# Optimization experiments

Measured on AMD Instinct MI355X. Metric: run time of the kernel, lower is better.

The kernel has to match this reference:

```python
import jax, jax.numpy as jnp
import numpy as np
import math

D_MODEL = 512


def setup_inputs() -> dict:
    key = jax.random.key(0)
    x = jax.random.normal(key, (16384, 32), dtype=jnp.float32)
    return {"x": x}


def reference(x) -> jnp.ndarray:
    # x: [B, F]; output: [B, D_MODEL]
    d_model = D_MODEL
    # div_term: [D/2]
    div_term = jnp.exp(jnp.arange(0, d_model, 2, dtype=jnp.float32) * (-(math.log(10000.0) / d_model)))
    # sinusoid input: [B, F, D/2]
    si = x[:, :, None] * div_term
    sin_mean = jnp.sin(si).mean(axis=1)  # [B, D/2]
    cos_mean = jnp.cos(si).mean(axis=1)  # [B, D/2]
    # interleave: out[:, 0::2] = sin_mean, out[:, 1::2] = cos_mean
    out = jnp.stack([sin_mean, cos_mean], axis=-1).reshape(x.shape[0], d_model)
    return out
```

## Files before the change

kernel.cpp:

```cpp
#include <hip/hip_runtime.h>

#define F 32
#define TPB 256
#define BLOCKS 2048

__device__ constexpr float kTable[14] = {
     3.125e-2f,
    -1.5625e-2f,
    -5.2083333333333e-3f,
     1.3020833333333e-3f,
     2.6041666666667e-4f,
    -4.3402777777778e-5f,
    -6.2003968253968e-6f,
     7.7504960317460e-7f,
     8.6116622574956e-8f,
    -8.6116622574956e-9f,
    -7.8287838704505e-10f,
     6.5239865587088e-11f,
     5.0184511989929e-12f,
    -3.5846079992806e-13f
};

#define DPP_ADD(x, ctrl)                                                                 \
    x += __int_as_float(__builtin_amdgcn_update_dpp(                                     \
        0, __float_as_int(x), (ctrl), 0xf, 0xf, true))

#define RDLANE(x, l) __int_as_float(__builtin_amdgcn_readlane(__float_as_int(x), (l)))

__global__ __launch_bounds__(TPB) void pe_kernel(const float* __restrict__ x,
                                                 float4* __restrict__ out,
                                                 int B) {
    const int lane = threadIdx.x & 63;
    const int fl   = lane & 31;
    const bool hi  = lane >= 32;
    const int gwave  = blockIdx.x * (TPB / 64) + (threadIdx.x >> 6);
    const int nwaves = gridDim.x * (TPB / 64);

    const float kExp = -0.05190512648261503f;

    float coef[7];
#pragma unroll
    for (int k = 0; k < 7; ++k) coef[k] = hi ? kTable[7 + k] : kTable[k];

    float d[4], t[4];
    d[0] = __builtin_amdgcn_exp2f((float)(2 * lane) * kExp);
    d[1] = __builtin_amdgcn_exp2f((float)(2 * lane + 1) * kExp);
    d[2] = d[0] * 0.01f;
    d[3] = d[1] * 0.01f;
#pragma unroll
    for (int m = 0; m < 4; ++m) t[m] = d[m] * d[m];

    for (int r = gwave; r < B; r += nwaves) {
        const float v = x[r * F + fl];
        const float v2 = v * v,   v3 = v2 * v,  v4 = v2 * v2,
                    v5 = v3 * v2, v6 = v3 * v3, v8 = v4 * v4;
        const float base = hi ? v8 : v;

        float rm[7];
        rm[0] = base * coef[0];
        rm[1] = (base * coef[1]) * v;
        rm[2] = (base * coef[2]) * v2;
        rm[3] = (base * coef[3]) * v3;
        rm[4] = (base * coef[4]) * v4;
        rm[5] = (base * coef[5]) * v5;
        rm[6] = (base * coef[6]) * v6;

#pragma unroll
        for (int k = 0; k < 7; ++k) {
            DPP_ADD(rm[k], 0x111);
            DPP_ADD(rm[k], 0x112);
            DPP_ADD(rm[k], 0x114);
            DPP_ADD(rm[k], 0x118);
            DPP_ADD(rm[k], 0x142);
        }

        const float M1  = RDLANE(rm[0], 31), M2  = RDLANE(rm[1], 31),
                    M3  = RDLANE(rm[2], 31), M4  = RDLANE(rm[3], 31),
                    M5  = RDLANE(rm[4], 31), M6  = RDLANE(rm[5], 31),
                    M7  = RDLANE(rm[6], 31),
                    M8  = RDLANE(rm[0], 63), M9  = RDLANE(rm[1], 63),
                    M10 = RDLANE(rm[2], 63), M11 = RDLANE(rm[3], 63),
                    M12 = RDLANE(rm[4], 63), M13 = RDLANE(rm[5], 63),
                    M14 = RDLANE(rm[6], 63);

        float4* orow = out + r * (512 / 4);
#pragma unroll
        for (int m = 0; m < 2; ++m) {
            const float ta = t[2 * m], tb = t[2 * m + 1];

            float s0 = M13;
            s0 = fmaf(s0, ta, M11); s0 = fmaf(s0, ta, M9);
            s0 = fmaf(s0, ta, M7);  s0 = fmaf(s0, ta, M5);
            s0 = fmaf(s0, ta, M3);  s0 = fmaf(s0, ta, M1);
            float c0 = M14;
            c0 = fmaf(c0, ta, M12); c0 = fmaf(c0, ta, M10);
            c0 = fmaf(c0, ta, M8);  c0 = fmaf(c0, ta, M6);
            c0 = fmaf(c0, ta, M4);  c0 = fmaf(c0, ta, M2);
            c0 = fmaf(c0, ta, 1.0f);

            float s1 = M13;
            s1 = fmaf(s1, tb, M11); s1 = fmaf(s1, tb, M9);
            s1 = fmaf(s1, tb, M7);  s1 = fmaf(s1, tb, M5);
            s1 = fmaf(s1, tb, M3);  s1 = fmaf(s1, tb, M1);
            float c1 = M14;
            c1 = fmaf(c1, tb, M12); c1 = fmaf(c1, tb, M10);
            c1 = fmaf(c1, tb, M8);  c1 = fmaf(c1, tb, M6);
            c1 = fmaf(c1, tb, M4);  c1 = fmaf(c1, tb, M2);
            c1 = fmaf(c1, tb, 1.0f);

            orow[lane + 64 * m] =
                make_float4(s0 * d[2 * m], c0, s1 * d[2 * m + 1], c1);
        }
    }
}

extern "C" void kernel_launch(void* const* d_in, const int* in_sizes, int n_in,
                              void* d_out, int out_size, void* d_ws, size_t ws_size,
                              hipStream_t stream) {
    const float* x = (const float*)d_in[0];
    float4* out = (float4*)d_out;
    const int B = in_sizes[0] / F;
    pe_kernel<<<BLOCKS, TPB, 0, stream>>>(x, out, B);
}
```

Before: 66.05 us.

## Use one wave per row, packed FMA Horner, and nontemporal stores

Replaces the grid-stride loop with one row per wave and doubles the block count to 4096 so the grid exactly covers B rows. The sin and cos Horner polynomials are paired into two-wide vector FMAs, which can map to packed FP32 FMA instructions. Output stores become nontemporal. The trade-off is that the per-lane setup (exp2 and coefficient selects) is now paid once per row instead of being amortized over several rows.

New measurement: 65.15 us. No clear change (-1.4%).

```diff
diff --git a/kernel.cpp b/kernel.cpp
--- a/kernel.cpp
+++ b/kernel.cpp
@@ -2,7 +2,10 @@
 
 #define F 32
 #define TPB 256
-#define BLOCKS 2048
+#define BLOCKS 4096
+
+typedef float f32x2 __attribute__((ext_vector_type(2)));
+typedef float f32x4 __attribute__((ext_vector_type(4)));
 
 __device__ constexpr float kTable[14] = {
      3.125e-2f,
@@ -28,13 +31,13 @@
 #define RDLANE(x, l) __int_as_float(__builtin_amdgcn_readlane(__float_as_int(x), (l)))
 
 __global__ __launch_bounds__(TPB) void pe_kernel(const float* __restrict__ x,
-                                                 float4* __restrict__ out,
+                                                 f32x4* __restrict__ out,
                                                  int B) {
     const int lane = threadIdx.x & 63;
     const int fl   = lane & 31;
     const bool hi  = lane >= 32;
-    const int gwave  = blockIdx.x * (TPB / 64) + (threadIdx.x >> 6);
-    const int nwaves = gridDim.x * (TPB / 64);
+    const int r    = blockIdx.x * (TPB / 64) + (threadIdx.x >> 6);
+    if (r >= B) return;
 
     const float kExp = -0.05190512648261503f;
 
@@ -50,67 +53,65 @@
 #pragma unroll
     for (int m = 0; m < 4; ++m) t[m] = d[m] * d[m];
 
-    for (int r = gwave; r < B; r += nwaves) {
-        const float v = x[r * F + fl];
-        const float v2 = v * v,   v3 = v2 * v,  v4 = v2 * v2,
-                    v5 = v3 * v2, v6 = v3 * v3, v8 = v4 * v4;
-        const float base = hi ? v8 : v;
+    const float v = x[r * F + fl];
+    const float v2 = v * v,   v3 = v2 * v,  v4 = v2 * v2,
+                v5 = v3 * v2, v6 = v3 * v3, v8 = v4 * v4;
+    const float base = hi ? v8 : v;
 
-        float rm[7];
-        rm[0] = base * coef[0];
-        rm[1] = (base * coef[1]) * v;
-        rm[2] = (base * coef[2]) * v2;
-        rm[3] = (base * coef[3]) * v3;
-        rm[4] = (base * coef[4]) * v4;
-        rm[5] = (base * coef[5]) * v5;
-        rm[6] = (base * coef[6]) * v6;
+    float rm[7];
+    rm[0] = base * coef[0];
+    rm[1] = (base * coef[1]) * v;
+    rm[2] = (base * coef[2]) * v2;
+    rm[3] = (base * coef[3]) * v3;
+    rm[4] = (base * coef[4]) * v4;
+    rm[5] = (base * coef[5]) * v5;
+    rm[6] = (base * coef[6]) * v6;
 
 #pragma unroll
-        for (int k = 0; k < 7; ++k) {
-            DPP_ADD(rm[k], 0x111);
-            DPP_ADD(rm[k], 0x112);
-            DPP_ADD(rm[k], 0x114);
-            DPP_ADD(rm[k], 0x118);
-            DPP_ADD(rm[k], 0x142);
-        }
+    for (int k = 0; k < 7; ++k) {
+        DPP_ADD(rm[k], 0x111);
+        DPP_ADD(rm[k], 0x112);
+        DPP_ADD(rm[k], 0x114);
+        DPP_ADD(rm[k], 0x118);
+        DPP_ADD(rm[k], 0x142);
+    }
 
-        const float M1  = RDLANE(rm[0], 31), M2  = RDLANE(rm[1], 31),
-                    M3  = RDLANE(rm[2], 31), M4  = RDLANE(rm[3], 31),
-                    M5  = RDLANE(rm[4], 31), M6  = RDLANE(rm[5], 31),
-                    M7  = RDLANE(rm[6], 31),
-                    M8  = RDLANE(rm[0], 63), M9  = RDLANE(rm[1], 63),
-                    M10 = RDLANE(rm[2], 63), M11 = RDLANE(rm[3], 63),
-                    M12 = RDLANE(rm[4], 63), M13 = RDLANE(rm[5], 63),
-                    M14 = RDLANE(rm[6], 63);
+    const f32x2 P1  = { RDLANE(rm[0], 31), RDLANE(rm[1], 31) };
+    const f32x2 P3  = { RDLANE(rm[2], 31), RDLANE(rm[3], 31) };
+    const f32x2 P5  = { RDLANE(rm[4], 31), RDLANE(rm[5], 31) };
+    const f32x2 P7  = { RDLANE(rm[6], 31), RDLANE(rm[0], 63) };
+    const f32x2 P9  = { RDLANE(rm[1], 63), RDLANE(rm[2], 63) };
+    const f32x2 P11 = { RDLANE(rm[3], 63), RDLANE(rm[4], 63) };
+    const f32x2 P13 = { RDLANE(rm[5], 63), RDLANE(rm[6], 63) };
 
-        float4* orow = out + r * (512 / 4);
+    f32x4* orow = out + r * (512 / 4);
 #pragma unroll
-        for (int m = 0; m < 2; ++m) {
-            const float ta = t[2 * m], tb = t[2 * m + 1];
+    for (int m = 0; m < 2; ++m) {
+        const float ta = t[2 * m], tb = t[2 * m + 1];
+        const f32x2 ta2 = {ta, ta}, tb2 = {tb, tb};
 
-            float s0 = M13;
-            s0 = fmaf(s0, ta, M11); s0 = fmaf(s0, ta, M9);
-            s0 = fmaf(s0, ta, M7);  s0 = fmaf(s0, ta, M5);
-            s0 = fmaf(s0, ta, M3);  s0 = fmaf(s0, ta, M1);
-            float c0 = M14;
-            c0 = fmaf(c0, ta, M12); c0 = fmaf(c0, ta, M10);
-            c0 = fmaf(c0, ta, M8);  c0 = fmaf(c0, ta, M6);
-            c0 = fmaf(c0, ta, M4);  c0 = fmaf(c0, ta, M2);
-            c0 = fmaf(c0, ta, 1.0f);
+        f32x2 a0 = P13;
+        a0 = __builtin_elementwise_fma(a0, ta2, P11);
+        a0 = __builtin_elementwise_fma(a0, ta2, P9);
+        a0 = __builtin_elementwise_fma(a0, ta2, P7);
+        a0 = __builtin_elementwise_fma(a0, ta2, P5);
+        a0 = __builtin_elementwise_fma(a0, ta2, P3);
+        a0 = __builtin_elementwise_fma(a0, ta2, P1);
+        const float s0 = a0.x;
+        const float c0 = fmaf(a0.y, ta, 1.0f);
 
-            float s1 = M13;
-            s1 = fmaf(s1, tb, M11); s1 = fmaf(s1, tb, M9);
-            s1 = fmaf(s1, tb, M7);  s1 = fmaf(s1, tb, M5);
-            s1 = fmaf(s1, tb, M3);  s1 = fmaf(s1, tb, M1);
-            float c1 = M14;
-            c1 = fmaf(c1, tb, M12); c1 = fmaf(c1, tb, M10);
-            c1 = fmaf(c1, tb, M8);  c1 = fmaf(c1, tb, M6);
-            c1 = fmaf(c1, tb, M4);  c1 = fmaf(c1, tb, M2);
-            c1 = fmaf(c1, tb, 1.0f);
+        f32x2 a1 = P13;
+        a1 = __builtin_elementwise_fma(a1, tb2, P11);
+        a1 = __builtin_elementwise_fma(a1, tb2, P9);
+        a1 = __builtin_elementwise_fma(a1, tb2, P7);
+        a1 = __builtin_elementwise_fma(a1, tb2, P5);
+        a1 = __builtin_elementwise_fma(a1, tb2, P3);
+        a1 = __builtin_elementwise_fma(a1, tb2, P1);
+        const float s1 = a1.x;
+        const float c1 = fmaf(a1.y, tb, 1.0f);
 
-            orow[lane + 64 * m] =
-                make_float4(s0 * d[2 * m], c0, s1 * d[2 * m + 1], c1);
-        }
+        const f32x4 res = {s0 * d[2 * m], c0, s1 * d[2 * m + 1], c1};
+        __builtin_nontemporal_store(res, &orow[lane + 64 * m]);
     }
 }
 
@@ -118,7 +119,7 @@
                               void* d_out, int out_size, void* d_ws, size_t ws_size,
                               hipStream_t stream) {
     const float* x = (const float*)d_in[0];
-    float4* out = (float4*)d_out;
+    f32x4* out = (f32x4*)d_out;
     const int B = in_sizes[0] / F;
     pe_kernel<<<BLOCKS, TPB, 0, stream>>>(x, out, B);
 }
```
